# Performance work log

Measured on AMD Instinct MI355X. Metric: run time of the kernel, lower is better.

The kernel has to match this reference:

```python
import jax, jax.numpy as jnp
import numpy as np

B, F_, P, C, H, W = 2048, 1024, 64, 1, 8, 8


def setup_inputs() -> dict:
    key = jax.random.key(0)
    k1, k2 = jax.random.split(key)
    x = jax.random.normal(k1, (B, C, H, W), dtype=jnp.float32)
    # sampled weights ww = sampler(get_features()): (out_dim, n_samples, *inp_shape)
    ww = jax.random.normal(k2, (F_, P, C, H, W), dtype=jnp.float32)
    scale = jnp.ones((1, F_), dtype=jnp.float32)
    bias = jnp.zeros((1, F_), dtype=jnp.float32)
    return {"x": x, "ww": ww, "scale": scale, "bias": bias}


def reference(x, ww, scale, bias):
    # x: (b, C, H, W) -> (b, i);  ww: (f, p, C, H, W) -> (f, p, i)
    xf = x.reshape(x.shape[0], -1)
    wwf = ww.reshape(ww.shape[0], ww.shape[1], -1)
    # scores: (b, p, f) -- the large intermediate a fused kernel would avoid
    scores = jnp.einsum('bi,fpi->bpf', xf, wwf)
    out = jnp.max(scores, axis=1)          # max-pool over samples p -> (b, f)
    out = out * scale + bias               # rescale=True, add_bias=True
    return out                             # act = Identity
```

## Files before the change

kernel.cpp:

```cpp
#include <hip/hip_runtime.h>

typedef __bf16 bf16x8 __attribute__((ext_vector_type(8)));
typedef __bf16 bf16x4 __attribute__((ext_vector_type(4)));
typedef float f32x16 __attribute__((ext_vector_type(16)));

constexpr int kB = 2048, kF = 1024, kP = 64, kK = 64;
constexpr int B_TILE = 256, F_TILE = 4;

__global__ __launch_bounds__(256, 2)
void affine_max_mfma(const float* __restrict__ x, const float* __restrict__ ww,
                     const float* __restrict__ scale, const float* __restrict__ bias,
                     float* __restrict__ out) {
  __shared__ __align__(16) char s_ww[F_TILE * kP * kK * 2];
  __shared__ __align__(16) char s_x[B_TILE * kK * 2];

  const int tid = threadIdx.x;
  const int bgroup = blockIdx.x >> 8;
  const int fgroup = blockIdx.x & 255;
  const int b0 = bgroup * B_TILE;
  const int f0 = fgroup * F_TILE;

  {
    const float* src = ww + (size_t)f0 * (kP * kK);
#pragma unroll
    for (int it = 0; it < 16; ++it) {
      const int e = it * 1024 + tid * 4;
      const float4 v = *reinterpret_cast<const float4*>(src + e);
      const int off = (e << 1) ^ (((e >> 6) & 7) << 4);
      bf16x4 h;
      h[0] = (__bf16)v.x; h[1] = (__bf16)v.y; h[2] = (__bf16)v.z; h[3] = (__bf16)v.w;
      *reinterpret_cast<bf16x4*>(s_ww + off) = h;
    }
  }
  {
    const float* src = x + (size_t)b0 * kK;
#pragma unroll
    for (int it = 0; it < 16; ++it) {
      const int e = it * 1024 + tid * 4;
      const float4 v = *reinterpret_cast<const float4*>(src + e);
      const int off = (e << 1) ^ (((e >> 6) & 7) << 4);
      bf16x4 h;
      h[0] = (__bf16)v.x; h[1] = (__bf16)v.y; h[2] = (__bf16)v.z; h[3] = (__bf16)v.w;
      *reinterpret_cast<bf16x4*>(s_x + off) = h;
    }
  }
  __syncthreads();

  const int wv = tid >> 6;
  const int lane = tid & 63;
  const int l31 = lane & 31;
  const int half = lane >> 5;
  const int f = f0 + wv;
  const float scl = scale[f];
  const float bia = bias[f];

  bf16x8 afr[2][4];
#pragma unroll
  for (int mt = 0; mt < 2; ++mt)
#pragma unroll
    for (int ks = 0; ks < 4; ++ks) {
      const int p = mt * 32 + l31;
      const int kb = ks * 16 + half * 8;
      const int off = ((wv * 4096 + p * 64 + kb) << 1) ^ ((p & 7) << 4);
      afr[mt][ks] = *reinterpret_cast<const bf16x8*>(s_ww + off);
    }

#pragma unroll
  for (int nt = 0; nt < 8; ++nt) {
    const int brow = nt * 32 + l31;
    bf16x8 bfr[4];
#pragma unroll
    for (int ks = 0; ks < 4; ++ks) {
      const int kb = ks * 16 + half * 8;
      const int off = ((brow * 64 + kb) << 1) ^ ((brow & 7) << 4);
      bfr[ks] = *reinterpret_cast<const bf16x8*>(s_x + off);
    }
    f32x16 acc0 = {}, acc1 = {};
#pragma unroll
    for (int ks = 0; ks < 4; ++ks) {
      acc0 = __builtin_amdgcn_mfma_f32_32x32x16_bf16(afr[0][ks], bfr[ks], acc0, 0, 0, 0);
      acc1 = __builtin_amdgcn_mfma_f32_32x32x16_bf16(afr[1][ks], bfr[ks], acc1, 0, 0, 0);
    }
    float v = -__builtin_inff();
#pragma unroll
    for (int i = 0; i < 16; ++i) v = fmaxf(v, fmaxf(acc0[i], acc1[i]));
    v = fmaxf(v, __shfl_xor(v, 32));
    if (lane < 32) out[(b0 + brow) * kF + f] = v * scl + bia;
  }
}

extern "C" void kernel_launch(void* const* d_in, const int* in_sizes, int n_in,
                              void* d_out, int out_size, void* d_ws, size_t ws_size,
                              hipStream_t stream) {
  const float* x = (const float*)d_in[0];
  const float* ww = (const float*)d_in[1];
  const float* scale = (const float*)d_in[2];
  const float* bias = (const float*)d_in[3];
  float* out = (float*)d_out;
  dim3 grid((kB / B_TILE) * (kF / F_TILE));
  dim3 block(256);
  hipLaunchKernelGGL(affine_max_mfma, grid, block, 0, stream,
                     x, ww, scale, bias, out);
}
```

Before: 101.6 us.

## Keep x fragments in registers and loop four F passes per block

Each block now covers 16 features instead of 4 and runs four passes over them. The x tile's bf16 fragments stay in registers across all passes, and ww is loaded straight from global into registers rather than staged through LDS. Outputs are gathered in LDS and written as coalesced float4 rows with scale and bias applied, and block indices are swizzled across feature chunks. This cuts redundant x loads, LDS traffic and scattered 4-byte stores, but raises register pressure (128 VGPRs for bfr alone) and loads ww uncoalesced per lane.

```diff
diff --git a/kernel.cpp b/kernel.cpp
--- a/kernel.cpp
+++ b/kernel.cpp
@@ -5,33 +5,23 @@
 typedef float f32x16 __attribute__((ext_vector_type(16)));
 
 constexpr int kB = 2048, kF = 1024, kP = 64, kK = 64;
-constexpr int B_TILE = 256, F_TILE = 4;
+constexpr int B_TILE = 256;
+constexpr int F_CHUNK = 16;
+constexpr int N_PASS = 4;
 
 __global__ __launch_bounds__(256, 2)
 void affine_max_mfma(const float* __restrict__ x, const float* __restrict__ ww,
                      const float* __restrict__ scale, const float* __restrict__ bias,
                      float* __restrict__ out) {
-  __shared__ __align__(16) char s_ww[F_TILE * kP * kK * 2];
-  __shared__ __align__(16) char s_x[B_TILE * kK * 2];
+  __shared__ __align__(16) char s_buf[32 * 1024];
 
   const int tid = threadIdx.x;
-  const int bgroup = blockIdx.x >> 8;
-  const int fgroup = blockIdx.x & 255;
+  const int bx = blockIdx.x;
+  const int fchunk = (bx & 7) * 8 + ((bx >> 3) & 7);
+  const int bgroup = bx >> 6;
   const int b0 = bgroup * B_TILE;
-  const int f0 = fgroup * F_TILE;
+  const int f0 = fchunk * F_CHUNK;
 
-  {
-    const float* src = ww + (size_t)f0 * (kP * kK);
-#pragma unroll
-    for (int it = 0; it < 16; ++it) {
-      const int e = it * 1024 + tid * 4;
-      const float4 v = *reinterpret_cast<const float4*>(src + e);
-      const int off = (e << 1) ^ (((e >> 6) & 7) << 4);
-      bf16x4 h;
-      h[0] = (__bf16)v.x; h[1] = (__bf16)v.y; h[2] = (__bf16)v.z; h[3] = (__bf16)v.w;
-      *reinterpret_cast<bf16x4*>(s_ww + off) = h;
-    }
-  }
   {
     const float* src = x + (size_t)b0 * kK;
 #pragma unroll
@@ -41,7 +31,7 @@
       const int off = (e << 1) ^ (((e >> 6) & 7) << 4);
       bf16x4 h;
       h[0] = (__bf16)v.x; h[1] = (__bf16)v.y; h[2] = (__bf16)v.z; h[3] = (__bf16)v.w;
-      *reinterpret_cast<bf16x4*>(s_x + off) = h;
+      *reinterpret_cast<bf16x4*>(s_buf + off) = h;
     }
   }
   __syncthreads();
@@ -50,42 +40,78 @@
   const int lane = tid & 63;
   const int l31 = lane & 31;
   const int half = lane >> 5;
-  const int f = f0 + wv;
-  const float scl = scale[f];
-  const float bia = bias[f];
 
-  bf16x8 afr[2][4];
-#pragma unroll
-  for (int mt = 0; mt < 2; ++mt)
-#pragma unroll
-    for (int ks = 0; ks < 4; ++ks) {
-      const int p = mt * 32 + l31;
-      const int kb = ks * 16 + half * 8;
-      const int off = ((wv * 4096 + p * 64 + kb) << 1) ^ ((p & 7) << 4);
-      afr[mt][ks] = *reinterpret_cast<const bf16x8*>(s_ww + off);
-    }
-
+  bf16x8 bfr[8][4];
 #pragma unroll
   for (int nt = 0; nt < 8; ++nt) {
     const int brow = nt * 32 + l31;
-    bf16x8 bfr[4];
 #pragma unroll
     for (int ks = 0; ks < 4; ++ks) {
       const int kb = ks * 16 + half * 8;
       const int off = ((brow * 64 + kb) << 1) ^ ((brow & 7) << 4);
-      bfr[ks] = *reinterpret_cast<const bf16x8*>(s_x + off);
+      bfr[nt][ks] = *reinterpret_cast<const bf16x8*>(s_buf + off);
     }
-    f32x16 acc0 = {}, acc1 = {};
+  }
+  __syncthreads();
+
+  float* s_out = reinterpret_cast<float*>(s_buf);
+
+#pragma unroll 1
+  for (int pass = 0; pass < N_PASS; ++pass) {
+    const int f = f0 + pass * 4 + wv;
+    bf16x8 afr[2][4];
 #pragma unroll
-    for (int ks = 0; ks < 4; ++ks) {
-      acc0 = __builtin_amdgcn_mfma_f32_32x32x16_bf16(afr[0][ks], bfr[ks], acc0, 0, 0, 0);
-      acc1 = __builtin_amdgcn_mfma_f32_32x32x16_bf16(afr[1][ks], bfr[ks], acc1, 0, 0, 0);
+    for (int mt = 0; mt < 2; ++mt) {
+      const int p = mt * 32 + l31;
+      const float* rowp = ww + (size_t)f * (kP * kK) + p * kK;
+#pragma unroll
+      for (int ks = 0; ks < 4; ++ks) {
+        const int kb = ks * 16 + half * 8;
+        const float4 lo = *reinterpret_cast<const float4*>(rowp + kb);
+        const float4 hi = *reinterpret_cast<const float4*>(rowp + kb + 4);
+        bf16x8 h;
+        h[0] = (__bf16)lo.x; h[1] = (__bf16)lo.y; h[2] = (__bf16)lo.z; h[3] = (__bf16)lo.w;
+        h[4] = (__bf16)hi.x; h[5] = (__bf16)hi.y; h[6] = (__bf16)hi.z; h[7] = (__bf16)hi.w;
+        afr[mt][ks] = h;
+      }
     }
-    float v = -__builtin_inff();
+
 #pragma unroll
-    for (int i = 0; i < 16; ++i) v = fmaxf(v, fmaxf(acc0[i], acc1[i]));
-    v = fmaxf(v, __shfl_xor(v, 32));
-    if (lane < 32) out[(b0 + brow) * kF + f] = v * scl + bia;
+    for (int nt = 0; nt < 8; ++nt) {
+      f32x16 acc0 = {}, acc1 = {};
+#pragma unroll
+      for (int ks = 0; ks < 4; ++ks) {
+        acc0 = __builtin_amdgcn_mfma_f32_32x32x16_bf16(afr[0][ks], bfr[nt][ks], acc0, 0, 0, 0);
+        acc1 = __builtin_amdgcn_mfma_f32_32x32x16_bf16(afr[1][ks], bfr[nt][ks], acc1, 0, 0, 0);
+      }
+      float a[16];
+#pragma unroll
+      for (int i = 0; i < 16; ++i) a[i] = fmaxf(acc0[i], acc1[i]);
+#pragma unroll
+      for (int s = 8; s >= 1; s >>= 1)
+#pragma unroll
+        for (int i = 0; i < s; ++i) a[i] = fmaxf(a[i], a[i + s]);
+      float v = fmaxf(a[0], __shfl_xor(a[0], 32));
+      if (lane < 32) s_out[(nt * 32 + l31) * 20 + pass * 4 + wv] = v;
+    }
+  }
+  __syncthreads();
+
+  {
+    const int q = tid & 3;
+    const float4 scl = *reinterpret_cast<const float4*>(scale + f0 + q * 4);
+    const float4 bia = *reinterpret_cast<const float4*>(bias + f0 + q * 4);
+#pragma unroll
+    for (int it = 0; it < 4; ++it) {
+      const int b = (tid >> 2) + it * 64;
+      const float4 vv = *reinterpret_cast<const float4*>(s_out + b * 20 + q * 4);
+      float4 r;
+      r.x = vv.x * scl.x + bia.x;
+      r.y = vv.y * scl.y + bia.y;
+      r.z = vv.z * scl.z + bia.z;
+      r.w = vv.w * scl.w + bia.w;
+      *reinterpret_cast<float4*>(out + (size_t)(b0 + b) * kF + f0 + q * 4) = r;
+    }
   }
 }
 
@@ -97,7 +123,7 @@
   const float* scale = (const float*)d_in[2];
   const float* bias = (const float*)d_in[3];
   float* out = (float*)d_out;
-  dim3 grid((kB / B_TILE) * (kF / F_TILE));
+  dim3 grid((kB / B_TILE) * (kF / F_CHUNK));
   dim3 block(256);
   hipLaunchKernelGGL(affine_max_mfma, grid, block, 0, stream,
                      x, ww, scale, bias, out);
```

After: 93.47 us. -8.0%, faster.

## Pre-pack inputs to MFMA fragment-order bf16 and restructure tiling with staged stores

Applied to the files above, without the earlier changes.

Adds a separate pack kernel that converts ww and x to bf16 in global workspace, laid out in the exact MFMA fragment order. The main kernel then loads fragments straight from global memory without going through LDS. The main kernel now covers 8 features by 512 batch rows per block, double-buffers the B-fragment loads, maps blocks to XCDs for locality, and stages results through LDS for coalesced float4 output stores. This cuts the redundant per-block fp32 conversion and LDS staging of ww and x, at the cost of a second launch and an extra workspace round trip.

```diff
diff --git a/kernel.cpp b/kernel.cpp
--- a/kernel.cpp
+++ b/kernel.cpp
@@ -1,91 +1,130 @@
 #include <hip/hip_runtime.h>
 
 typedef __bf16 bf16x8 __attribute__((ext_vector_type(8)));
-typedef __bf16 bf16x4 __attribute__((ext_vector_type(4)));
 typedef float f32x16 __attribute__((ext_vector_type(16)));
 
 constexpr int kB = 2048, kF = 1024, kP = 64, kK = 64;
-constexpr int B_TILE = 256, F_TILE = 4;
+constexpr size_t WWPK_BYTES = (size_t)kF * kP * kK * 2;
+
+
+__global__ __launch_bounds__(256, 8)
+void pack_kernel(const float* __restrict__ x, const float* __restrict__ ww,
+                 __bf16* __restrict__ wwpk, __bf16* __restrict__ xpk) {
+  const int bx = blockIdx.x, tid = threadIdx.x;
+  if (bx < 2048) {
+    const int g = bx * 256 + tid;
+    const float4 lo = *reinterpret_cast<const float4*>(ww + (size_t)g * 8);
+    const float4 hi = *reinterpret_cast<const float4*>(ww + (size_t)g * 8 + 4);
+    const int f = g >> 9, rem = g & 511;
+    const int p = rem >> 3, k8 = rem & 7;
+    const int ks = k8 >> 1, half = k8 & 1, mt = p >> 5, p31 = p & 31;
+    const int chunk = ((f * 4 + ks) * 2 + half) * 64 + mt * 32 + p31;
+    bf16x8 h;
+    h[0] = (__bf16)lo.x; h[1] = (__bf16)lo.y; h[2] = (__bf16)lo.z; h[3] = (__bf16)lo.w;
+    h[4] = (__bf16)hi.x; h[5] = (__bf16)hi.y; h[6] = (__bf16)hi.z; h[7] = (__bf16)hi.w;
+    *reinterpret_cast<bf16x8*>(wwpk + (size_t)chunk * 8) = h;
+  } else {
+    const int g = (bx - 2048) * 256 + tid;
+    const float4 lo = *reinterpret_cast<const float4*>(x + (size_t)g * 8);
+    const float4 hi = *reinterpret_cast<const float4*>(x + (size_t)g * 8 + 4);
+    const int b = g >> 3, k8 = g & 7;
+    const int bt = b >> 5, b31 = b & 31;
+    const int chunk = (bt * 8 + k8) * 32 + b31;
+    bf16x8 h;
+    h[0] = (__bf16)lo.x; h[1] = (__bf16)lo.y; h[2] = (__bf16)lo.z; h[3] = (__bf16)lo.w;
+    h[4] = (__bf16)hi.x; h[5] = (__bf16)hi.y; h[6] = (__bf16)hi.z; h[7] = (__bf16)hi.w;
+    *reinterpret_cast<bf16x8*>(xpk + (size_t)chunk * 8) = h;
+  }
+}
 
 __global__ __launch_bounds__(256, 2)
-void affine_max_mfma(const float* __restrict__ x, const float* __restrict__ ww,
+void affine_max_mfma(const __bf16* __restrict__ wwpk, const __bf16* __restrict__ xpk,
                      const float* __restrict__ scale, const float* __restrict__ bias,
                      float* __restrict__ out) {
-  __shared__ __align__(16) char s_ww[F_TILE * kP * kK * 2];
-  __shared__ __align__(16) char s_x[B_TILE * kK * 2];
+  __shared__ float s_out[512 * 10];
 
-  const int tid = threadIdx.x;
-  const int bgroup = blockIdx.x >> 8;
-  const int fgroup = blockIdx.x & 255;
-  const int b0 = bgroup * B_TILE;
-  const int f0 = fgroup * F_TILE;
+  const int tid = threadIdx.x, bx = blockIdx.x;
+  const int xcd = bx & 7, j = bx >> 3;
+  const int fchunk = xcd * 16 + (j & 15);
+  const int bgroup = j >> 4;
+  const int f0 = fchunk * 8;
+  const int b0 = bgroup * 512;
 
-  {
-    const float* src = ww + (size_t)f0 * (kP * kK);
+  const int wv = tid >> 6, lane = tid & 63, l31 = lane & 31, half = lane >> 5;
+
+  const char* wbase = reinterpret_cast<const char*>(wwpk) + half * 1024 + l31 * 16;
+  bf16x8 afr[2][2][4];
 #pragma unroll
-    for (int it = 0; it < 16; ++it) {
-      const int e = it * 1024 + tid * 4;
-      const float4 v = *reinterpret_cast<const float4*>(src + e);
-      const int off = (e << 1) ^ (((e >> 6) & 7) << 4);
-      bf16x4 h;
-      h[0] = (__bf16)v.x; h[1] = (__bf16)v.y; h[2] = (__bf16)v.z; h[3] = (__bf16)v.w;
-      *reinterpret_cast<bf16x4*>(s_ww + off) = h;
+  for (int fi = 0; fi < 2; ++fi) {
+    const size_t fb = (size_t)(f0 + wv * 2 + fi) * 8192;
+#pragma unroll
+    for (int mt = 0; mt < 2; ++mt)
+#pragma unroll
+      for (int ks = 0; ks < 4; ++ks)
+        afr[fi][mt][ks] =
+            *reinterpret_cast<const bf16x8*>(wbase + fb + ks * 2048 + mt * 512);
+  }
+
+  const char* xbase = reinterpret_cast<const char*>(xpk) +
+                      (size_t)(bgroup * 16) * 4096 + half * 512 + l31 * 16;
+  auto loadB = [&](int t, bf16x8 (&dst)[4]) {
+#pragma unroll
+    for (int ks = 0; ks < 4; ++ks)
+      dst[ks] = *reinterpret_cast<const bf16x8*>(xbase + t * 4096 + ks * 1024);
+  };
+  auto compute = [&](int t, bf16x8 (&bfr)[4]) {
+    f32x16 acc[2][2] = {};
+#pragma unroll
+    for (int ks = 0; ks < 4; ++ks)
+#pragma unroll
+      for (int fi = 0; fi < 2; ++fi)
+#pragma unroll
+        for (int mt = 0; mt < 2; ++mt)
+          acc[fi][mt] = __builtin_amdgcn_mfma_f32_32x32x16_bf16(
+              afr[fi][mt][ks], bfr[ks], acc[fi][mt], 0, 0, 0);
+#pragma unroll
+    for (int fi = 0; fi < 2; ++fi) {
+      float a[16];
+#pragma unroll
+      for (int i = 0; i < 16; ++i) a[i] = fmaxf(acc[fi][0][i], acc[fi][1][i]);
+#pragma unroll
+      for (int s = 8; s >= 1; s >>= 1)
+#pragma unroll
+        for (int i = 0; i < s; ++i) a[i] = fmaxf(a[i], a[i + s]);
+      const float v = fmaxf(a[0], __shfl_xor(a[0], 32));
+      if (lane < 32) s_out[(t * 32 + l31) * 10 + wv * 2 + fi] = v;
     }
+  };
+
+  bf16x8 bA[4], bB[4];
+  loadB(0, bA);
+#pragma unroll 1
+  for (int t = 0; t < 14; t += 2) {
+    loadB(t + 1, bB);
+    compute(t, bA);
+    loadB(t + 2, bA);
+    compute(t + 1, bB);
   }
-  {
-    const float* src = x + (size_t)b0 * kK;
-#pragma unroll
-    for (int it = 0; it < 16; ++it) {
-      const int e = it * 1024 + tid * 4;
-      const float4 v = *reinterpret_cast<const float4*>(src + e);
-      const int off = (e << 1) ^ (((e >> 6) & 7) << 4);
-      bf16x4 h;
-      h[0] = (__bf16)v.x; h[1] = (__bf16)v.y; h[2] = (__bf16)v.z; h[3] = (__bf16)v.w;
-      *reinterpret_cast<bf16x4*>(s_x + off) = h;
-    }
-  }
+  loadB(15, bB);
+  compute(14, bA);
+  compute(15, bB);
+
   __syncthreads();
 
-  const int wv = tid >> 6;
-  const int lane = tid & 63;
-  const int l31 = lane & 31;
-  const int half = lane >> 5;
-  const int f = f0 + wv;
-  const float scl = scale[f];
-  const float bia = bias[f];
-
-  bf16x8 afr[2][4];
+  const int c4 = (tid & 1) * 4;
+  const float4 scl = *reinterpret_cast<const float4*>(scale + f0 + c4);
+  const float4 bia = *reinterpret_cast<const float4*>(bias + f0 + c4);
 #pragma unroll
-  for (int mt = 0; mt < 2; ++mt)
-#pragma unroll
-    for (int ks = 0; ks < 4; ++ks) {
-      const int p = mt * 32 + l31;
-      const int kb = ks * 16 + half * 8;
-      const int off = ((wv * 4096 + p * 64 + kb) << 1) ^ ((p & 7) << 4);
-      afr[mt][ks] = *reinterpret_cast<const bf16x8*>(s_ww + off);
-    }
-
-#pragma unroll
-  for (int nt = 0; nt < 8; ++nt) {
-    const int brow = nt * 32 + l31;
-    bf16x8 bfr[4];
-#pragma unroll
-    for (int ks = 0; ks < 4; ++ks) {
-      const int kb = ks * 16 + half * 8;
-      const int off = ((brow * 64 + kb) << 1) ^ ((brow & 7) << 4);
-      bfr[ks] = *reinterpret_cast<const bf16x8*>(s_x + off);
-    }
-    f32x16 acc0 = {}, acc1 = {};
-#pragma unroll
-    for (int ks = 0; ks < 4; ++ks) {
-      acc0 = __builtin_amdgcn_mfma_f32_32x32x16_bf16(afr[0][ks], bfr[ks], acc0, 0, 0, 0);
-      acc1 = __builtin_amdgcn_mfma_f32_32x32x16_bf16(afr[1][ks], bfr[ks], acc1, 0, 0, 0);
-    }
-    float v = -__builtin_inff();
-#pragma unroll
-    for (int i = 0; i < 16; ++i) v = fmaxf(v, fmaxf(acc0[i], acc1[i]));
-    v = fmaxf(v, __shfl_xor(v, 32));
-    if (lane < 32) out[(b0 + brow) * kF + f] = v * scl + bia;
+  for (int i = 0; i < 4; ++i) {
+    const int row = i * 128 + (tid >> 1);
+    const float2 u0 = *reinterpret_cast<const float2*>(&s_out[row * 10 + c4]);
+    const float2 u1 = *reinterpret_cast<const float2*>(&s_out[row * 10 + c4 + 2]);
+    float4 r;
+    r.x = u0.x * scl.x + bia.x;
+    r.y = u0.y * scl.y + bia.y;
+    r.z = u1.x * scl.z + bia.z;
+    r.w = u1.y * scl.w + bia.w;
+    *reinterpret_cast<float4*>(out + (size_t)(b0 + row) * kF + f0 + c4) = r;
   }
 }
 
@@ -97,8 +136,11 @@
   const float* scale = (const float*)d_in[2];
   const float* bias = (const float*)d_in[3];
   float* out = (float*)d_out;
-  dim3 grid((kB / B_TILE) * (kF / F_TILE));
-  dim3 block(256);
-  hipLaunchKernelGGL(affine_max_mfma, grid, block, 0, stream,
-                     x, ww, scale, bias, out);
+  __bf16* wwpk = (__bf16*)d_ws;
+  __bf16* xpk = (__bf16*)((char*)d_ws + WWPK_BYTES);
+
+  hipLaunchKernelGGL(pack_kernel, dim3(2048 + 64), dim3(256), 0, stream,
+                     x, ww, wwpk, xpk);
+  hipLaunchKernelGGL(affine_max_mfma, dim3(512), dim3(256), 0, stream,
+                     wwpk, xpk, scale, bias, out);
 }
```

New measurement: 91.27 us. 10.2% less time.
